# Optimization experiments

Hardware: AMD Instinct MI355X
Metric: run time of the kernel (lower is better)

## Reference

```python
import jax, jax.numpy as jnp
import numpy as np

IN_DIM, OUT_DIM = 32, 16
NUM_BINS, EMBED, HEADS = 1100, 8, 4
MN, MX = -1.0, 300.0
BATCH = 1024


def setup_inputs() -> dict:
    key = jax.random.key(0)
    ks = jax.random.split(key, 8)
    s = 1.0 / np.sqrt(EMBED)
    x = jax.random.uniform(ks[0], (BATCH, IN_DIM), jnp.float32, MN, MX)
    emb = jax.random.normal(ks[1], (IN_DIM, NUM_BINS, EMBED), jnp.float32)  # per-feature tables
    in_proj_w = jax.random.uniform(ks[2], (3 * EMBED, EMBED), jnp.float32, -s, s)
    in_proj_b = jnp.zeros((3 * EMBED,), jnp.float32)
    out_proj_w = jax.random.uniform(ks[3], (EMBED, EMBED), jnp.float32, -s, s)
    out_proj_b = jnp.zeros((EMBED,), jnp.float32)
    sl = 1.0 / np.sqrt(IN_DIM * EMBED)
    lin_w = jax.random.uniform(ks[4], (OUT_DIM, IN_DIM * EMBED), jnp.float32, -sl, sl)
    lin_b = jax.random.uniform(ks[5], (OUT_DIM,), jnp.float32, -sl, sl)
    return {"x": x, "emb": emb, "in_proj_w": in_proj_w, "in_proj_b": in_proj_b,
            "out_proj_w": out_proj_w, "out_proj_b": out_proj_b,
            "lin_w": lin_w, "lin_b": lin_b}


def reference(x, emb, in_proj_w, in_proj_b, out_proj_w, out_proj_b, lin_w, lin_b):
    B, F = x.shape
    H, hd = HEADS, EMBED // HEADS
    # clamp + bucketize (torch.bucketize right=False == searchsorted side='left')
    bins = jnp.linspace(MN, MX, NUM_BINS)
    idx = jnp.searchsorted(bins, jnp.clip(x, MN, MX), side="left")  # (B, F)
    # per-feature embedding gather
    xe = emb[jnp.arange(F)[None, :], idx]  # (B, F, E)
    # MultiheadAttention with batch_first=False: seq axis = B, batch axis = F
    Wq, Wk, Wv = jnp.split(in_proj_w, 3, axis=0)
    bq, bk, bv = jnp.split(in_proj_b, 3)
    q = (xe @ Wq.T + bq).reshape(B, F, H, hd)
    k = (xe @ Wk.T + bk).reshape(B, F, H, hd)
    v = (xe @ Wv.T + bv).reshape(B, F, H, hd)
    scores = jnp.einsum("bfhd,cfhd->fhbc", q, k) / np.sqrt(hd)  # (F, H, B, B)
    attn = jax.nn.softmax(scores, axis=-1)
    o = jnp.einsum("fhbc,cfhd->bfhd", attn, v).reshape(B, F, EMBED)
    o = o @ out_proj_w.T + out_proj_b  # (B, F, E)
    logits = o.reshape(B, F * EMBED) @ lin_w.T + lin_b  # (B, OUT_DIM)
    return jax.nn.softmax(logits, axis=-1)
```

## Files before the change

kernel.cpp:

```cpp
#include <hip/hip_runtime.h>
#include <math.h>

#define NF 32
#define NB 1100
#define NE 8
#define NH 4
#define NBATCH 1024
#define NFH 128

__device__ __forceinline__ float fexp2(float x){
#if __has_builtin(__builtin_amdgcn_exp2f)
  return __builtin_amdgcn_exp2f(x);
#else
  return exp2f(x);
#endif
}

__device__ __forceinline__ double bin_at(int i){
  #pragma clang fp contract(off)
  const double step = 301.0 / 1099.0;
  if (i == NB - 1) return 300.0;
  return (double)i * step + (-1.0);
}

__global__ __launch_bounds__(256) void k1_embed_qkv(
    const float* __restrict__ x, const float* __restrict__ emb,
    const float* __restrict__ W, const float* __restrict__ bias,
    float* __restrict__ q_ws, float* __restrict__ kv_ws)
{
  __shared__ float sW[192];
  __shared__ float sB[24];
  const int tid = threadIdx.x;
  if (tid < 192) sW[tid] = W[tid];
  if (tid < 24)  sB[tid] = bias[tid];
  __syncthreads();

  const int f = blockIdx.y;
  const int b = blockIdx.x * 256 + tid;

  float xv = x[b * NF + f];
  xv = fminf(fmaxf(xv, -1.0f), 300.0f);
  const double xd = (double)xv;

  int lo = 0, hi = NB;
  while (lo < hi) {
    const int mid = (lo + hi) >> 1;
    if (bin_at(mid) < xd) lo = mid + 1; else hi = mid;
  }
  const int idx = lo;

  const float4* ep = (const float4*)(emb + ((size_t)f * NB + idx) * NE);
  const float4 e0 = ep[0], e1 = ep[1];
  const float xe[8] = {e0.x, e0.y, e0.z, e0.w, e1.x, e1.y, e1.z, e1.w};

  float qv[8], kv[8], vv[8];
  #pragma unroll
  for (int i = 0; i < 8; ++i) { qv[i] = sB[i]; kv[i] = sB[8+i]; vv[i] = sB[16+i]; }
  #pragma unroll
  for (int j = 0; j < 8; ++j) {
    const float xj = xe[j];
    #pragma unroll
    for (int i = 0; i < 8; ++i) {
      qv[i] = fmaf(xj, sW[      i*8 + j], qv[i]);
      kv[i] = fmaf(xj, sW[ 64 + i*8 + j], kv[i]);
      vv[i] = fmaf(xj, sW[128 + i*8 + j], vv[i]);
    }
  }

  const float QS = (float)(1.4426950408889634 / 1.4142135623730951);
  float2* qp = (float2*)q_ws;
  float4* kvp = (float4*)kv_ws;
  #pragma unroll
  for (int h = 0; h < NH; ++h) {
    const int fh = f * NH + h;
    qp [fh * NBATCH + b] = make_float2(qv[2*h] * QS, qv[2*h+1] * QS);
    kvp[fh * NBATCH + b] = make_float4(kv[2*h], kv[2*h+1], vv[2*h], vv[2*h+1]);
  }
}

__global__ __launch_bounds__(512) void k2_attn(
    const float* __restrict__ q_ws, const float* __restrict__ kv_ws,
    float* __restrict__ o_ws)
{
  __shared__ float4 skv[NBATCH];
  __shared__ float sred[8];
  __shared__ float sl[256], so0[256], so1[256];
  const int tid = threadIdx.x;
  const int fh = blockIdx.y;

  const float4* kvg = (const float4*)kv_ws + (size_t)fh * NBATCH;
  const float4 t0 = kvg[tid], t1 = kvg[tid + 512];
  skv[tid] = t0;
  skv[tid + 512] = t1;
  float mx2 = fmaxf(fmaf(t0.x, t0.x, t0.y * t0.y), fmaf(t1.x, t1.x, t1.y * t1.y));
  #pragma unroll
  for (int off = 32; off >= 1; off >>= 1)
    mx2 = fmaxf(mx2, __shfl_xor(mx2, off, 64));
  if ((tid & 63) == 0) sred[tid >> 6] = mx2;
  __syncthreads();
  float Mn2 = sred[0];
  #pragma unroll
  for (int w = 1; w < 8; ++w) Mn2 = fmaxf(Mn2, sred[w]);
  const float Mn = sqrtf(Mn2);

  const int qi = tid & 255;
  const int half = tid >> 8;
  const int b = blockIdx.x * 256 + qi;
  const float2 q = ((const float2*)q_ws)[(size_t)fh * NBATCH + b];
  const float negm = -sqrtf(fmaf(q.x, q.x, q.y * q.y)) * Mn;

  float l = 0.0f, o0 = 0.0f, o1 = 0.0f;
  const int c0 = half << 9;
  #pragma unroll 8
  for (int c = 0; c < 512; ++c) {
    const float4 kv = skv[c0 + c];
    const float s = fmaf(q.x, kv.x, fmaf(q.y, kv.y, negm));
    const float p = fexp2(s);
    l += p;
    o0 = fmaf(p, kv.z, o0);
    o1 = fmaf(p, kv.w, o1);
  }
  if (half == 1) { sl[qi] = l; so0[qi] = o0; so1[qi] = o1; }
  __syncthreads();
  if (half == 0) {
    l += sl[qi]; o0 += so0[qi]; o1 += so1[qi];
    const float inv = 1.0f / l;
    ((float2*)o_ws)[(size_t)fh * NBATCH + b] = make_float2(o0 * inv, o1 * inv);
  }
}

__global__ __launch_bounds__(256) void k3_final(
    const float* __restrict__ o_ws, const float* __restrict__ opw,
    const float* __restrict__ opb,  const float* __restrict__ lw,
    const float* __restrict__ lb,   float* __restrict__ out)
{
  __shared__ float sWc[4096];
  __shared__ float sbc[16];
  __shared__ float sWo[64];
  const int tid = threadIdx.x;
  if (tid < 64) sWo[tid] = opw[tid];
  __syncthreads();
  #pragma unroll
  for (int i = tid; i < 4096; i += 256) {
    const int t = i >> 8, fe = i & 255;
    const int f8 = fe & ~7, e2 = fe & 7;
    float acc = 0.0f;
    #pragma unroll
    for (int e = 0; e < 8; ++e) acc = fmaf(lw[t*256 + f8 + e], sWo[e*8 + e2], acc);
    sWc[i] = acc;
  }
  {
    const int t = tid >> 4, seg = tid & 15;
    float acc = 0.0f;
    #pragma unroll
    for (int j = 0; j < 16; ++j) {
      const int fe = seg * 16 + j;
      acc = fmaf(lw[t*256 + fe], opb[fe & 7], acc);
    }
    #pragma unroll
    for (int off = 8; off >= 1; off >>= 1) acc += __shfl_xor(acc, off, 64);
    if (seg == 0) sbc[t] = acc + lb[t];
  }
  __syncthreads();

  const int gid = blockIdx.x * 256 + tid;
  const int b = gid >> 4;
  const int t = gid & 15;
  const float2* op = (const float2*)o_ws;
  const float2* wp = (const float2*)sWc + t * 128;
  float acc = sbc[t];
  #pragma unroll 8
  for (int fh = 0; fh < NFH; ++fh) {
    const float2 ov = op[(size_t)fh * NBATCH + b];
    const float2 wv = wp[fh];
    acc = fmaf(ov.x, wv.x, fmaf(ov.y, wv.y, acc));
  }
  float mx = acc;
  #pragma unroll
  for (int off = 8; off >= 1; off >>= 1) mx = fmaxf(mx, __shfl_xor(mx, off, 64));
  const float p = expf(acc - mx);
  float s = p;
  #pragma unroll
  for (int off = 8; off >= 1; off >>= 1) s += __shfl_xor(s, off, 64);
  out[gid] = p / s;
}

extern "C" void kernel_launch(void* const* d_in, const int* in_sizes, int n_in,
                              void* d_out, int out_size, void* d_ws, size_t ws_size,
                              hipStream_t stream)
{
  const float* x   = (const float*)d_in[0];
  const float* emb = (const float*)d_in[1];
  const float* ipw = (const float*)d_in[2];
  const float* ipb = (const float*)d_in[3];
  const float* opw = (const float*)d_in[4];
  const float* opb = (const float*)d_in[5];
  const float* lw  = (const float*)d_in[6];
  const float* lb  = (const float*)d_in[7];

  float* ws    = (float*)d_ws;
  float* q_ws  = ws;
  float* kv_ws = ws + 262144;
  float* o_ws  = ws + 786432;

  k1_embed_qkv<<<dim3(4, NF), 256, 0, stream>>>(x, emb, ipw, ipb, q_ws, kv_ws);
  k2_attn<<<dim3(4, NFH), 512, 0, stream>>>(q_ws, kv_ws, o_ws);
  k3_final<<<64, 256, 0, stream>>>(o_ws, opw, opb, lw, lb, (float*)d_out);
}
```

Before: 109.7 us.

## Split K/V into paired shared arrays for packed-FP32 attention loop

The attention kernel now stores keys and values in separate shared arrays, interleaving pairs of keys, so each loop step handles two keys with 2-wide vector math that can map to packed FP32 instructions. The inner loop runs half as many iterations, and the reduction order of the softmax sums changes. The embed/QKV kernel also moves to 128-thread blocks with twice as many blocks, to spread across more compute units. The packed form targets the FMA and add cost around the exp2 bottleneck, but exp2 itself stays scalar.

```diff
diff --git a/kernel.cpp b/kernel.cpp
--- a/kernel.cpp
+++ b/kernel.cpp
@@ -8,6 +8,8 @@
 #define NBATCH 1024
 #define NFH 128
 
+typedef float vf2 __attribute__((ext_vector_type(2)));
+
 __device__ __forceinline__ float fexp2(float x){
 #if __has_builtin(__builtin_amdgcn_exp2f)
   return __builtin_amdgcn_exp2f(x);
@@ -23,7 +25,7 @@
   return (double)i * step + (-1.0);
 }
 
-__global__ __launch_bounds__(256) void k1_embed_qkv(
+__global__ __launch_bounds__(128) void k1_embed_qkv(
     const float* __restrict__ x, const float* __restrict__ emb,
     const float* __restrict__ W, const float* __restrict__ bias,
     float* __restrict__ q_ws, float* __restrict__ kv_ws)
@@ -31,12 +33,12 @@
   __shared__ float sW[192];
   __shared__ float sB[24];
   const int tid = threadIdx.x;
-  if (tid < 192) sW[tid] = W[tid];
+  for (int i = tid; i < 192; i += 128) sW[i] = W[i];
   if (tid < 24)  sB[tid] = bias[tid];
   __syncthreads();
 
   const int f = blockIdx.y;
-  const int b = blockIdx.x * 256 + tid;
+  const int b = blockIdx.x * 128 + tid;
 
   float xv = x[b * NF + f];
   xv = fminf(fmaxf(xv, -1.0f), 300.0f);
@@ -82,17 +84,18 @@
     const float* __restrict__ q_ws, const float* __restrict__ kv_ws,
     float* __restrict__ o_ws)
 {
-  __shared__ float4 skv[NBATCH];
+  __shared__ float4 skk[512];
+  __shared__ float4 svv[512];
   __shared__ float sred[8];
   __shared__ float sl[256], so0[256], so1[256];
   const int tid = threadIdx.x;
   const int fh = blockIdx.y;
 
   const float4* kvg = (const float4*)kv_ws + (size_t)fh * NBATCH;
-  const float4 t0 = kvg[tid], t1 = kvg[tid + 512];
-  skv[tid] = t0;
-  skv[tid + 512] = t1;
-  float mx2 = fmaxf(fmaf(t0.x, t0.x, t0.y * t0.y), fmaf(t1.x, t1.x, t1.y * t1.y));
+  const float4 a0 = kvg[2*tid], a1 = kvg[2*tid+1];
+  skk[tid] = make_float4(a0.x, a1.x, a0.y, a1.y);
+  svv[tid] = make_float4(a0.z, a1.z, a0.w, a1.w);
+  float mx2 = fmaxf(fmaf(a0.x, a0.x, a0.y * a0.y), fmaf(a1.x, a1.x, a1.y * a1.y));
   #pragma unroll
   for (int off = 32; off >= 1; off >>= 1)
     mx2 = fmaxf(mx2, __shfl_xor(mx2, off, 64));
@@ -109,17 +112,26 @@
   const float2 q = ((const float2*)q_ws)[(size_t)fh * NBATCH + b];
   const float negm = -sqrtf(fmaf(q.x, q.x, q.y * q.y)) * Mn;
 
-  float l = 0.0f, o0 = 0.0f, o1 = 0.0f;
-  const int c0 = half << 9;
+  const vf2 qxx = {q.x, q.x};
+  const vf2 qyy = {q.y, q.y};
+  const vf2 nm2 = {negm, negm};
+  vf2 lp = {0.0f, 0.0f}, o0p = {0.0f, 0.0f}, o1p = {0.0f, 0.0f};
+
+  const int p0 = half << 8;
   #pragma unroll 8
-  for (int c = 0; c < 512; ++c) {
-    const float4 kv = skv[c0 + c];
-    const float s = fmaf(q.x, kv.x, fmaf(q.y, kv.y, negm));
-    const float p = fexp2(s);
-    l += p;
-    o0 = fmaf(p, kv.z, o0);
-    o1 = fmaf(p, kv.w, o1);
-  }
+  for (int i = 0; i < 256; ++i) {
+    const float4 kk = skk[p0 + i];
+    const float4 vv = svv[p0 + i];
+    const vf2 k0p = {kk.x, kk.y}, k1p = {kk.z, kk.w};
+    const vf2 v0p = {vv.x, vv.y}, v1p = {vv.z, vv.w};
+    const vf2 s = qxx * k0p + qyy * k1p + nm2;
+    vf2 pp; pp.x = fexp2(s.x); pp.y = fexp2(s.y);
+    lp  += pp;
+    o0p += pp * v0p;
+    o1p += pp * v1p;
+  }
+  float l = lp.x + lp.y, o0 = o0p.x + o0p.y, o1 = o1p.x + o1p.y;
+
   if (half == 1) { sl[qi] = l; so0[qi] = o0; so1[qi] = o1; }
   __syncthreads();
   if (half == 0) {
@@ -203,7 +215,7 @@
   float* kv_ws = ws + 262144;
   float* o_ws  = ws + 786432;
 
-  k1_embed_qkv<<<dim3(4, NF), 256, 0, stream>>>(x, emb, ipw, ipb, q_ws, kv_ws);
+  k1_embed_qkv<<<dim3(8, NF), 128, 0, stream>>>(x, emb, ipw, ipb, q_ws, kv_ws);
   k2_attn<<<dim3(4, NFH), 512, 0, stream>>>(q_ws, kv_ws, o_ws);
   k3_final<<<64, 256, 0, stream>>>(o_ws, opw, opb, lw, lb, (float*)d_out);
 }
```

New measurement: 109.2 us. About the same (-0.5%).
